# Performance work log

Measured on AMD Instinct MI355X. Metric: run time of the kernel, lower is better.

## Reference

```python
import jax, jax.numpy as jnp
import numpy as np

N_LEVELS = 16
F_PER_LEVEL = 2
T = 1 << 19  # hashmap size per level
BASE_RES = 16
DST_RES = 4096
B = float(np.exp(np.log(DST_RES / BASE_RES) / (N_LEVELS - 1)))  # per-level scale
MOVING_STEP = 1.0 / 4096.0
AABB_MIN = -1.5
AABB_MAX = 1.5
GEO_FEAT_DIM = 15
CORNERS = np.array([[i, j, k] for i in (0, 1) for j in (0, 1) for k in (0, 1)], dtype=np.int32)  # [8,3]
PRIMES = np.array([1, 2654435761, 805459861], dtype=np.uint32)


def mlp(h, Ws):
    # tcnn FullyFusedMLP: bias-free linear layers, ReLU hidden, linear output
    for W in Ws[:-1]:
        h = jax.nn.relu(h @ W)
    return h @ Ws[-1]


def freq_encode(x, n_freqs):
    # tcnn Frequency encoding: sin/cos(2^f * pi * x) per dim/freq; [N,D] -> [N, D*n_freqs*2]
    f = (2.0 ** jnp.arange(n_freqs, dtype=jnp.float32)) * jnp.pi
    xf = x[..., None] * f  # [N, D, nf]
    return jnp.concatenate([jnp.sin(xf), jnp.cos(xf)], axis=-1).reshape(x.shape[0], -1)


def sh_encode_deg4(d):
    # real spherical harmonics, degree 4 (16 coeffs), unit direction input
    x, y, z = d[..., 0], d[..., 1], d[..., 2]
    xy, yz, xz = x * y, y * z, x * z
    x2, y2, z2 = x * x, y * y, z * z
    return jnp.stack([
        0.28209479177387814 * jnp.ones_like(x),
        -0.48860251190291987 * y,
        0.48860251190291987 * z,
        -0.48860251190291987 * x,
        1.0925484305920792 * xy,
        -1.0925484305920792 * yz,
        0.94617469575755997 * z2 - 0.31539156525251999,
        -1.0925484305920792 * xz,
        0.54627421529603959 * (x2 - y2),
        0.59004358992664352 * y * (y2 - 3.0 * x2),
        2.8906114426405538 * xy * z,
        0.45704579946446572 * y * (1.0 - 5.0 * z2),
        0.3731763325901154 * z * (5.0 * z2 - 3.0),
        0.45704579946446572 * x * (1.0 - 5.0 * z2),
        1.4453057213202769 * z * (x2 - y2),
        0.59004358992664352 * x * (3.0 * y2 - x2),
    ], axis=-1)  # [N,16]


def hash_encode(x, tables):
    # x: [N,3] in [0,1]; tables: [L, T, F]. Multi-res grid w/ trilinear interp;
    # dense indexing for small levels, spatial hashing for large ones (tcnn semantics).
    outs = []
    for l in range(N_LEVELS):
        scale = BASE_RES * (B ** l) - 1.0
        res = int(np.ceil(scale)) + 1
        pos = x * scale + 0.5
        pos0 = jnp.floor(pos)
        frac = pos - pos0
        c = pos0.astype(jnp.int32)[:, None, :] + CORNERS[None]  # [N,8,3]
        if res ** 3 <= T:
            idx = c[..., 0] + res * (c[..., 1] + res * c[..., 2])
        else:
            cu = c.astype(jnp.uint32)
            idx = (cu[..., 0] * PRIMES[0]) ^ (cu[..., 1] * PRIMES[1]) ^ (cu[..., 2] * PRIMES[2])
            idx = (idx % np.uint32(T)).astype(jnp.int32)
        feats = tables[l][idx]  # [N,8,F] gather
        w = jnp.prod(jnp.where(CORNERS[None] == 1, frac[:, None, :], 1.0 - frac[:, None, :]), axis=-1)  # [N,8]
        outs.append(jnp.einsum('ncf,nc->nf', feats, w))
    return jnp.concatenate(outs, axis=-1)  # [N, L*F]


def _w(k, fan_in, fan_out):
    return jax.random.normal(k, (fan_in, fan_out), jnp.float32) / np.sqrt(fan_in)


def setup_inputs() -> dict:
    key = jax.random.key(0)
    ks = jax.random.split(key, 12)
    N = 524288
    positions = jax.random.uniform(ks[0], (N, 3), jnp.float32, -1.2, 1.2)
    t = jax.random.uniform(ks[1], (N, 1), jnp.float32)
    directions = jax.random.normal(ks[2], (N, 3), jnp.float32)
    tables = jax.random.uniform(ks[3], (N_LEVELS, T, F_PER_LEVEL), jnp.float32, -1e-4, 1e-4)
    return {
        'positions': positions, 't': t, 'directions': directions, 'tables': tables,
        'w_wrap0': _w(ks[4], 32, 64), 'w_wrap1': _w(ks[5], 64, 64), 'w_wrap2': _w(ks[6], 64, 3),
        'w_base0': _w(ks[7], 32, 64), 'w_base1': _w(ks[8], 64, 1 + GEO_FEAT_DIM),
        'w_head0': _w(ks[9], 16 + GEO_FEAT_DIM, 64), 'w_head1': _w(ks[10], 64, 64), 'w_head2': _w(ks[11], 64, 3),
    }


def reference(positions, t, directions, tables,
              w_wrap0, w_wrap1, w_wrap2, w_base0, w_base1,
              w_head0, w_head1, w_head2):
    # query_move: frequency-encode (x,t), tiny MLP -> offsets, scaled by MOVING_STEP
    enc = freq_encode(jnp.concatenate([positions, t], axis=-1), 4)  # [N,32]
    offsets = mlp(enc, [w_wrap0, w_wrap1, w_wrap2])  # [N,3]
    x_move = positions + offsets * MOVING_STEP
    # normalize to aabb unit cube
    xn = (x_move - AABB_MIN) / (AABB_MAX - AABB_MIN)
    selector = jnp.all((xn > 0.0) & (xn < 1.0), axis=-1)
    hash_feat = hash_encode(xn, tables)  # [N,32]
    base = mlp(hash_feat, [w_base0, w_base1])  # [N,16]
    density = jnp.exp(base[:, :1] - 1.0) * selector[:, None].astype(base.dtype)  # trunc_exp(x-1)
    geo = base[:, 1:]
    dirs = directions / jnp.linalg.norm(directions, axis=-1, keepdims=True)
    sh = sh_encode_deg4(dirs)  # [N,16]
    rgb = jax.nn.sigmoid(mlp(jnp.concatenate([sh, geo], axis=-1), [w_head0, w_head1, w_head2]))
    return jnp.concatenate([rgb, density], axis=-1)  # [N,4] = (rgb, density)
```

## Files before the change

### kernel.cpp

```cpp
#include <hip/hip_runtime.h>
#include <math.h>

#define TPB   128
#define HTPB  256
#define HPTS  4
#define CHUNK 32
#define LDW   68
constexpr int  N_LVL = 16;
constexpr unsigned TBL = 1u << 19;
constexpr float MOVE_STEP = 1.0f / 4096.0f;

typedef __attribute__((ext_vector_type(8))) short short8;
typedef __attribute__((ext_vector_type(4))) float f32x4;

struct LevelParams { float scale[N_LVL]; int res[N_LVL]; int dense[N_LVL]; };

enum { C_W0 = 0, C_W1 = 4, C_W2 = 12, C_B0 = 14, C_B1 = 18, C_H0 = 20, C_H1 = 24, C_H2 = 32, C_TOT = 34 };

struct LayerDesc { const float* W; int K; int N; int ksteps; int ntiles; int cbase; };
struct AllLayers { LayerDesc L[8]; };

__device__ __forceinline__ unsigned short f2bf(float x) {
    unsigned int u = __float_as_uint(x);
    u += 0x7FFFu + ((u >> 16) & 1u);
    return (unsigned short)(u >> 16);
}
__device__ __forceinline__ float bf2f(unsigned short h) {
    return __uint_as_float(((unsigned int)h) << 16);
}
__device__ __forceinline__ unsigned pk(unsigned short a, unsigned short b) {
    return (unsigned)a | ((unsigned)b << 16);
}

__device__ __forceinline__ unsigned cvt_pk_bf16(float a, float b) {
    unsigned r;
    asm("v_cvt_pk_bf16_f32 %0, %1, %2" : "=v"(r) : "v"(a), "v"(b));
    return r;
}
__device__ __forceinline__ void split_pair(float a, float b, unsigned& hp, unsigned& lp) {
    hp = cvt_pk_bf16(a, b);
    const float ha = __uint_as_float(hp << 16);
    const float hb = __uint_as_float(hp & 0xffff0000u);
    lp = cvt_pk_bf16(a - ha, b - hb);
}

__global__ __launch_bounds__(256) void k_prep(AllLayers al, unsigned short* __restrict__ wfrag)
{
    const LayerDesc d = al.L[blockIdx.x];
    const int total = d.ksteps * d.ntiles * 64;
    for (int slot = threadIdx.x; slot < total; slot += 256) {
        const int lane = slot & 63;
        const int c = slot >> 6;
        const int s = c / d.ntiles;
        const int t = c - s * d.ntiles;
        short8 hv, lv;
#pragma unroll
        for (int j = 0; j < 8; ++j) {
            const int k = s * 32 + ((lane >> 4) << 3) + j;
            const int n = t * 16 + (lane & 15);
            const float w = (k < d.K && n < d.N) ? d.W[k * d.N + n] : 0.f;
            const unsigned short hi = f2bf(w);
            const unsigned short lo = f2bf(w - bf2f(hi));
            hv[j] = (short)hi;
            lv[j] = (short)lo;
        }
        short8* b8 = reinterpret_cast<short8*>(wfrag + (size_t)(d.cbase + c) * 1024);
        b8[lane]      = hv;
        b8[64 + lane] = lv;
    }
}

__global__ __launch_bounds__(256) void k_tab16(
    const float* __restrict__ g_tab, unsigned* __restrict__ tab16,
    int n_dense, int n_hashed)
{
    const size_t total_pairs = (size_t)n_hashed * (TBL / 2);
    const size_t gstride = (size_t)gridDim.x * 256;
    const float* __restrict__ src = g_tab + (size_t)n_dense * (TBL * 2);
    for (size_t i = (size_t)blockIdx.x * 256 + threadIdx.x; i < total_pairs; i += gstride) {
        const f32x4 v = reinterpret_cast<const f32x4*>(src)[i];
        uint2 o;
        o.x = pk(f2bf(v[0]), f2bf(v[1]));
        o.y = pk(f2bf(v[2]), f2bf(v[3]));
        reinterpret_cast<uint2*>(tab16)[i] = o;
    }
}

template<int KSTEPS, int NTILES, bool RELU>
__device__ __forceinline__ void wave_layer(float* X,
                                           const unsigned short* __restrict__ wfrag, int cbase,
                                           int wrow, int lane)
{
    f32x4 acc[2][NTILES];
#pragma unroll
    for (int ms = 0; ms < 2; ++ms)
#pragma unroll
        for (int t = 0; t < NTILES; ++t) acc[ms][t] = f32x4{0.f, 0.f, 0.f, 0.f};
    const int r15 = lane & 15, q = lane >> 4;
    const short8* wf8 = reinterpret_cast<const short8*>(wfrag) + (size_t)cbase * 128;
#pragma unroll
    for (int s = 0; s < KSTEPS; ++s) {
        short8 ah[2], al[2];
#pragma unroll
        for (int ms = 0; ms < 2; ++ms) {
            const float* xp = X + (size_t)(wrow + ms * 16 + r15) * LDW + s * 32 + q * 8;
            const f32x4 x0 = reinterpret_cast<const f32x4*>(xp)[0];
            const f32x4 x1 = reinterpret_cast<const f32x4*>(xp)[1];
            union { unsigned u[4]; short8 s8; } uh, ul;
            split_pair(x0[0], x0[1], uh.u[0], ul.u[0]);
            split_pair(x0[2], x0[3], uh.u[1], ul.u[1]);
            split_pair(x1[0], x1[1], uh.u[2], ul.u[2]);
            split_pair(x1[2], x1[3], uh.u[3], ul.u[3]);
            ah[ms] = uh.s8;
            al[ms] = ul.s8;
        }
#pragma unroll
        for (int t = 0; t < NTILES; ++t) {
            const short8* cp = wf8 + (size_t)(s * NTILES + t) * 128;
            const short8 bh = cp[lane];
            const short8 bl = cp[64 + lane];
#pragma unroll
            for (int ms = 0; ms < 2; ++ms) {
                acc[ms][t] = __builtin_amdgcn_mfma_f32_16x16x32_bf16(ah[ms], bh, acc[ms][t], 0, 0, 0);
                acc[ms][t] = __builtin_amdgcn_mfma_f32_16x16x32_bf16(al[ms], bh, acc[ms][t], 0, 0, 0);
                acc[ms][t] = __builtin_amdgcn_mfma_f32_16x16x32_bf16(ah[ms], bl, acc[ms][t], 0, 0, 0);
            }
        }
    }
#pragma unroll
    for (int ms = 0; ms < 2; ++ms)
#pragma unroll
        for (int t = 0; t < NTILES; ++t)
#pragma unroll
            for (int r = 0; r < 4; ++r) {
                float v = acc[ms][t][r];
                if (RELU) v = fmaxf(v, 0.f);
                X[(size_t)(wrow + ms * 16 + q * 4 + r) * LDW + t * 16 + r15] = v;
            }
}

__global__ __launch_bounds__(256, 4) void k_warp_mfma(
    const float* __restrict__ g_pos, const float* __restrict__ g_t,
    const float* __restrict__ g_tab,
    const unsigned short* __restrict__ wfrag,
    float* __restrict__ xn4,
    unsigned* __restrict__ featp, size_t stride, int N, int n_dense, LevelParams lp)
{
    __shared__ float buf[128 * LDW];
    const int tid = threadIdx.x;
    const int base = blockIdx.x * 128;
    const int p = tid & 127;
    const int pn = min(base + p, N - 1);
    const float PI_F = 3.14159265358979323846f;

    {
        const int dpair = tid >> 7;
        float v0, v1;
        if (dpair == 0) { v0 = g_pos[3 * pn + 0]; v1 = g_pos[3 * pn + 1]; }
        else            { v0 = g_pos[3 * pn + 2]; v1 = g_t[pn]; }
#pragma unroll
        for (int e = 0; e < 2; ++e) {
            const float x = e ? v1 : v0;
            const int d = dpair * 2 + e;
            f32x4 sv, cv;
#pragma unroll
            for (int k = 0; k < 4; ++k) {
                const float a = x * (PI_F * (float)(1 << k));
                sv[k] = __sinf(a);
                cv[k] = __cosf(a);
            }
            *reinterpret_cast<f32x4*>(&buf[(size_t)p * LDW + d * 8])     = sv;
            *reinterpret_cast<f32x4*>(&buf[(size_t)p * LDW + d * 8 + 4]) = cv;
        }
    }
    __syncthreads();
    const int lane = tid & 63, wrow = (tid >> 6) * 32;
    wave_layer<1, 4, true >(buf, wfrag, C_W0, wrow, lane);
    wave_layer<2, 4, true >(buf, wfrag, C_W1, wrow, lane);
    wave_layer<2, 1, false>(buf, wfrag, C_W2, wrow, lane);
    __syncthreads();

    const int n = base + p;
    const float ox = buf[(size_t)p * LDW + 0];
    const float oy = buf[(size_t)p * LDW + 1];
    const float oz = buf[(size_t)p * LDW + 2];
    const float xnv[3] = { (g_pos[3 * pn + 0] + ox * MOVE_STEP + 1.5f) / 3.0f,
                           (g_pos[3 * pn + 1] + oy * MOVE_STEP + 1.5f) / 3.0f,
                           (g_pos[3 * pn + 2] + oz * MOVE_STEP + 1.5f) / 3.0f };
    if (tid < 128 && n < N) {
        reinterpret_cast<f32x4*>(xn4)[n] = f32x4{ xnv[0], xnv[1], xnv[2], 0.f };
    }

    const int dmid = min(3, n_dense);
    const int l0 = (tid < 128) ? 0 : dmid;
    const int l1 = (tid < 128) ? dmid : n_dense;
    for (int l = l0; l < l1; ++l) {
        const float scale = lp.scale[l];
        const int res = lp.res[l];
        float fr[3]; int c0[3];
#pragma unroll
        for (int d = 0; d < 3; ++d) {
            const float pp = xnv[d] * scale + 0.5f;
            const float fl = floorf(pp);
            fr[d] = pp - fl;
            c0[d] = (int)fl;
        }
        const float* __restrict__ tbl = g_tab + (size_t)l * (size_t)(TBL * 2);
        float2 v[8];
#pragma unroll
        for (int c = 0; c < 8; ++c) {
            const int ci = (c >> 2) & 1, cj = (c >> 1) & 1, ck = c & 1;
            const unsigned idx = (unsigned)((c0[0] + ci) + res * ((c0[1] + cj) + res * (c0[2] + ck)));
            v[c] = *reinterpret_cast<const float2*>(tbl + (size_t)idx * 2);
        }
        float f0 = 0.f, f1 = 0.f;
#pragma unroll
        for (int c = 0; c < 8; ++c) {
            const int ci = (c >> 2) & 1, cj = (c >> 1) & 1, ck = c & 1;
            const float w = (ci ? fr[0] : 1.f - fr[0])
                          * (cj ? fr[1] : 1.f - fr[1])
                          * (ck ? fr[2] : 1.f - fr[2]);
            f0 = fmaf(w, v[c].x, f0);
            f1 = fmaf(w, v[c].y, f1);
        }
        if (n < N) {
            __builtin_nontemporal_store(pk(f2bf(f0), f2bf(f1)), &featp[(size_t)l * stride + n]);
        }
    }
}

__global__ __launch_bounds__(HTPB) void k_hash_all16(
    const unsigned* __restrict__ tab16,
    const float* __restrict__ xn4,
    unsigned* __restrict__ featp, size_t stride, int N, int n_dense, LevelParams lp)
{
    const int l = n_dense + blockIdx.y;
    const float scale = lp.scale[l];
    const unsigned* __restrict__ tbl = tab16 + (size_t)blockIdx.y * TBL;
    unsigned* __restrict__ op = featp + (size_t)l * stride;

    const int base = blockIdx.x * (HTPB * HPTS) + threadIdx.x;

    int nn[HPTS]; bool av[HPTS];
    f32x4 xs[HPTS];
#pragma unroll
    for (int k = 0; k < HPTS; ++k) {
        nn[k] = base + k * HTPB;
        av[k] = nn[k] < N;
        const int m = av[k] ? nn[k] : 0;
        xs[k] = reinterpret_cast<const f32x4*>(xn4)[m];
    }

    float frx[HPTS];
    float wyz[HPTS][4];
    uint2 w2[HPTS][4];
    unsigned vodd[HPTS][4] = {};
    unsigned ahi[HPTS];
    bool oddx[HPTS];
#pragma unroll
    for (int k = 0; k < HPTS; ++k) {
        int c0[3]; float fr[3];
#pragma unroll
        for (int d = 0; d < 3; ++d) {
            const float pp = xs[k][d] * scale + 0.5f;
            const float fl = floorf(pp);
            fr[d] = pp - fl;
            c0[d] = (int)fl;
        }
        frx[k] = fr[0];
        const unsigned ux  = (unsigned)c0[0];
        const unsigned ry0 = (unsigned)c0[1] * 2654435761u;
        const unsigned ry1 = (unsigned)(c0[1] + 1) * 2654435761u;
        const unsigned rz0 = (unsigned)c0[2] * 805459861u;
        const unsigned rz1 = (unsigned)(c0[2] + 1) * 805459861u;
        oddx[k] = (c0[0] & 1) != 0;
        const float wy0 = 1.f - fr[1], wy1 = fr[1];
        const float wz0 = 1.f - fr[2], wz1 = fr[2];
        wyz[k][0] = wy0 * wz0; wyz[k][1] = wy0 * wz1;
        wyz[k][2] = wy1 * wz0; wyz[k][3] = wy1 * wz1;
        const unsigned rr[4] = { ry0 ^ rz0, ry0 ^ rz1, ry1 ^ rz0, ry1 ^ rz1 };
        unsigned hb = 0;
#pragma unroll
        for (int pc = 0; pc < 4; ++pc) {
            const unsigned iA = (ux ^ rr[pc]) & (TBL - 1u);
            hb |= (iA & 1u) << pc;
            w2[k][pc] = *reinterpret_cast<const uint2*>(tbl + (iA & ~1u));
        }
        ahi[k] = hb;
        if (oddx[k]) {
#pragma unroll
            for (int pc = 0; pc < 4; ++pc) {
                const unsigned iB = ((ux + 1u) ^ rr[pc]) & (TBL - 1u);
                vodd[k][pc] = tbl[iB];
            }
        }
    }

#pragma unroll
    for (int k = 0; k < HPTS; ++k) {
        float f0 = 0.f, f1 = 0.f;
        const float wx0 = 1.f - frx[k], wx1 = frx[k];
#pragma unroll
        for (int pc = 0; pc < 4; ++pc) {
            const unsigned lo = w2[k][pc].x, hi = w2[k][pc].y;
            const bool a_hi = ((ahi[k] >> pc) & 1u) != 0;
            const unsigned vA = a_hi ? hi : lo;
            const unsigned vB = oddx[k] ? vodd[k][pc] : (a_hi ? lo : hi);
            const float wA = wx0 * wyz[k][pc];
            const float wB = wx1 * wyz[k][pc];
            f0 = fmaf(wA, bf2f((unsigned short)(vA & 0xffffu)), f0);
            f1 = fmaf(wA, bf2f((unsigned short)(vA >> 16)), f1);
            f0 = fmaf(wB, bf2f((unsigned short)(vB & 0xffffu)), f0);
            f1 = fmaf(wB, bf2f((unsigned short)(vB >> 16)), f1);
        }
        if (av[k]) __builtin_nontemporal_store(pk(f2bf(f0), f2bf(f1)), &op[nn[k]]);
    }
}

__global__ __launch_bounds__(256, 4) void k_final_mfma(
    const unsigned* __restrict__ featp, size_t stride,
    const float* __restrict__ xn4,
    const float* __restrict__ g_dir,
    const unsigned short* __restrict__ wfrag,
    float* __restrict__ g_out, int N)
{
    __shared__ float buf[128 * LDW];
    const int tid = threadIdx.x;
    const int base = blockIdx.x * 128;
    const int p = tid & 127;
    const int pn = min(base + p, N - 1);
    const int g = tid >> 7;

#pragma unroll
    for (int j = 0; j < 8; ++j) {
        const int l = g * 8 + j;
        const unsigned v = __builtin_nontemporal_load(&featp[(size_t)l * stride + pn]);
        buf[(size_t)p * LDW + 2 * l]     = bf2f((unsigned short)(v & 0xffffu));
        buf[(size_t)p * LDW + 2 * l + 1] = bf2f((unsigned short)(v >> 16));
    }
    __syncthreads();

    const int lane = tid & 63, wrow = (tid >> 6) * 32;
    wave_layer<1, 4, true >(buf, wfrag, C_B0, wrow, lane);
    wave_layer<2, 1, false>(buf, wfrag, C_B1, wrow, lane);
    __syncthreads();

    float density = 0.f;
    if (tid < 128) {
        float bb[16];
        const f32x4* bv = reinterpret_cast<const f32x4*>(&buf[(size_t)tid * LDW]);
#pragma unroll
        for (int g4 = 0; g4 < 4; ++g4) {
            const f32x4 v = bv[g4];
#pragma unroll
            for (int j = 0; j < 4; ++j) bb[4 * g4 + j] = v[j];
        }
        const f32x4 xv = reinterpret_cast<const f32x4*>(xn4)[pn];
        const bool sel = xv[0] > 0.f && xv[0] < 1.f && xv[1] > 0.f && xv[1] < 1.f &&
                         xv[2] > 0.f && xv[2] < 1.f;
        density = sel ? expf(bb[0] - 1.0f) : 0.0f;

        const float ddx = g_dir[3 * pn + 0];
        const float ddy = g_dir[3 * pn + 1];
        const float ddz = g_dir[3 * pn + 2];
        const float nrm = sqrtf(ddx * ddx + ddy * ddy + ddz * ddz);
        const float x = ddx / nrm, y = ddy / nrm, z = ddz / nrm;
        const float xy = x * y, yz = y * z, xz = x * z;
        const float x2 = x * x, y2 = y * y, z2 = z * z;
        f32x4 o0, o1, o2, o3, o4, o5, o6, o7;
        o0[0] = 0.28209479177387814f;
        o0[1] = -0.48860251190291987f * y;
        o0[2] = 0.48860251190291987f * z;
        o0[3] = -0.48860251190291987f * x;
        o1[0] = 1.0925484305920792f * xy;
        o1[1] = -1.0925484305920792f * yz;
        o1[2] = 0.94617469575756f * z2 - 0.31539156525252f;
        o1[3] = -1.0925484305920792f * xz;
        o2[0] = 0.5462742152960396f * (x2 - y2);
        o2[1] = 0.5900435899266435f * y * (y2 - 3.0f * x2);
        o2[2] = 2.890611442640554f * xy * z;
        o2[3] = 0.4570457994644657f * y * (1.0f - 5.0f * z2);
        o3[0] = 0.3731763325901154f * z * (5.0f * z2 - 3.0f);
        o3[1] = 0.4570457994644657f * x * (1.0f - 5.0f * z2);
        o3[2] = 1.445305721320277f * z * (x2 - y2);
        o3[3] = 0.5900435899266435f * x * (3.0f * y2 - x2);
        o4[0] = bb[1];  o4[1] = bb[2];  o4[2] = bb[3];  o4[3] = bb[4];
        o5[0] = bb[5];  o5[1] = bb[6];  o5[2] = bb[7];  o5[3] = bb[8];
        o6[0] = bb[9];  o6[1] = bb[10]; o6[2] = bb[11]; o6[3] = bb[12];
        o7[0] = bb[13]; o7[1] = bb[14]; o7[2] = bb[15]; o7[3] = 0.f;
        f32x4* wb = reinterpret_cast<f32x4*>(&buf[(size_t)tid * LDW]);
        wb[0] = o0; wb[1] = o1; wb[2] = o2; wb[3] = o3;
        wb[4] = o4; wb[5] = o5; wb[6] = o6; wb[7] = o7;
    }
    __syncthreads();

    wave_layer<1, 4, true >(buf, wfrag, C_H0, wrow, lane);
    wave_layer<2, 4, true >(buf, wfrag, C_H1, wrow, lane);
    wave_layer<2, 1, false>(buf, wfrag, C_H2, wrow, lane);
    __syncthreads();

    if (tid < 128 && base + tid < N) {
        const int n = base + tid;
        float4 o;
        o.x = 1.0f / (1.0f + expf(-buf[(size_t)tid * LDW + 0]));
        o.y = 1.0f / (1.0f + expf(-buf[(size_t)tid * LDW + 1]));
        o.z = 1.0f / (1.0f + expf(-buf[(size_t)tid * LDW + 2]));
        o.w = density;
        *reinterpret_cast<float4*>(g_out + (size_t)n * 4) = o;
    }
}

template<int IN, int OUT, bool RELU>
__device__ __forceinline__ void layer(const float* __restrict__ W,
                                      const float* __restrict__ hin,
                                      float* __restrict__ A,
                                      float* __restrict__ out)
{
#pragma unroll
    for (int j = 0; j < OUT; ++j) out[j] = 0.f;
#pragma unroll
    for (int c = 0; c < IN; c += CHUNK) {
#pragma unroll
        for (int i = 0; i < CHUNK; ++i) {
            if (c + i < IN) A[i * TPB] = RELU ? fmaxf(hin[c + i], 0.f) : hin[c + i];
        }
        const int cnt = (IN - c < CHUNK) ? (IN - c) : CHUNK;
#pragma unroll 4
        for (int i = 0; i < cnt; ++i) {
            const float a = A[i * TPB];
            const float* __restrict__ Wr = W + (size_t)(c + i) * OUT;
#pragma unroll
            for (int j = 0; j < OUT; ++j)
                out[j] = fmaf(a, Wr[j], out[j]);
        }
    }
}

__global__ __launch_bounds__(TPB, 4) void dngp_mono(
    const float* __restrict__ g_pos, const float* __restrict__ g_t,
    const float* __restrict__ g_dir, const float* __restrict__ g_tab,
    const float* __restrict__ Ww0, const float* __restrict__ Ww1, const float* __restrict__ Ww2,
    const float* __restrict__ Wb0, const float* __restrict__ Wb1,
    const float* __restrict__ Wh0, const float* __restrict__ Wh1, const float* __restrict__ Wh2,
    float* __restrict__ g_out, int N, LevelParams lp)
{
    __shared__ float s_act[CHUNK * TPB];
    const int tid = threadIdx.x;
    const int n = blockIdx.x * TPB + tid;
    if (n >= N) return;
    float* __restrict__ A = s_act + tid;

    const float px = g_pos[3 * n + 0];
    const float py = g_pos[3 * n + 1];
    const float pz = g_pos[3 * n + 2];
    const float tt = g_t[n];

    float enc[32];
    {
        const float xin[4] = { px, py, pz, tt };
        const float PI_F = 3.14159265358979323846f;
#pragma unroll
        for (int d = 0; d < 4; ++d)
#pragma unroll
            for (int k = 0; k < 4; ++k) {
                float s, c;
                sincosf(xin[d] * (PI_F * (float)(1 << k)), &s, &c);
                enc[d * 8 + k]     = s;
                enc[d * 8 + 4 + k] = c;
            }
    }

    float h[64], h2[64], off[3];
    layer<32, 64, false>(Ww0, enc, A, h);
    layer<64, 64, true >(Ww1, h,   A, h2);
    layer<64, 3,  true >(Ww2, h2,  A, off);

    const float xn[3] = { (px + off[0] * MOVE_STEP + 1.5f) / 3.0f,
                          (py + off[1] * MOVE_STEP + 1.5f) / 3.0f,
                          (pz + off[2] * MOVE_STEP + 1.5f) / 3.0f };
    const bool sel = xn[0] > 0.f && xn[0] < 1.f && xn[1] > 0.f && xn[1] < 1.f &&
                     xn[2] > 0.f && xn[2] < 1.f;

    float feat[32];
#pragma unroll 2
    for (int l = 0; l < N_LVL; ++l) {
        const float scale = lp.scale[l];
        const int res = lp.res[l];
        float fr[3]; int c0[3];
#pragma unroll
        for (int d = 0; d < 3; ++d) {
            const float pp = xn[d] * scale + 0.5f;
            const float fl = floorf(pp);
            fr[d] = pp - fl;
            c0[d] = (int)fl;
        }
        const float* __restrict__ tbl = g_tab + (size_t)l * (size_t)(TBL * 2);
        float f0 = 0.f, f1 = 0.f;
        if (lp.dense[l]) {
#pragma unroll
            for (int c = 0; c < 8; ++c) {
                const int ci = (c >> 2) & 1, cj = (c >> 1) & 1, ck = c & 1;
                const unsigned idx = (unsigned)((c0[0] + ci) + res * ((c0[1] + cj) + res * (c0[2] + ck)));
                const float2 f = *reinterpret_cast<const float2*>(tbl + (size_t)idx * 2);
                const float w = (ci ? fr[0] : 1.f - fr[0]) * (cj ? fr[1] : 1.f - fr[1]) * (ck ? fr[2] : 1.f - fr[2]);
                f0 = fmaf(w, f.x, f0);
                f1 = fmaf(w, f.y, f1);
            }
        } else {
#pragma unroll
            for (int c = 0; c < 8; ++c) {
                const int ci = (c >> 2) & 1, cj = (c >> 1) & 1, ck = c & 1;
                const unsigned hx = (unsigned)(c0[0] + ci);
                const unsigned hy = (unsigned)(c0[1] + cj) * 2654435761u;
                const unsigned hz = (unsigned)(c0[2] + ck) * 805459861u;
                const unsigned idx = (hx ^ hy ^ hz) & (TBL - 1u);
                const float2 f = *reinterpret_cast<const float2*>(tbl + (size_t)idx * 2);
                const float w = (ci ? fr[0] : 1.f - fr[0]) * (cj ? fr[1] : 1.f - fr[1]) * (ck ? fr[2] : 1.f - fr[2]);
                f0 = fmaf(w, f.x, f0);
                f1 = fmaf(w, f.y, f1);
            }
        }
        feat[2 * l]     = f0;
        feat[2 * l + 1] = f1;
    }

    layer<32, 64, false>(Wb0, feat, A, h);
    float b[16];
    layer<64, 16, true >(Wb1, h, A, b);
    const float density = sel ? expf(b[0] - 1.0f) : 0.0f;

    float hin[31];
    {
        const float ddx = g_dir[3 * n + 0];
        const float ddy = g_dir[3 * n + 1];
        const float ddz = g_dir[3 * n + 2];
        const float nrm = sqrtf(ddx * ddx + ddy * ddy + ddz * ddz);
        const float x = ddx / nrm, y = ddy / nrm, z = ddz / nrm;
        const float xy = x * y, yz = y * z, xz = x * z;
        const float x2_ = x * x, y2 = y * y, z2 = z * z;
        hin[0]  = 0.28209479177387814f;
        hin[1]  = -0.48860251190291987f * y;
        hin[2]  = 0.48860251190291987f * z;
        hin[3]  = -0.48860251190291987f * x;
        hin[4]  = 1.0925484305920792f * xy;
        hin[5]  = -1.0925484305920792f * yz;
        hin[6]  = 0.94617469575756f * z2 - 0.31539156525252f;
        hin[7]  = -1.0925484305920792f * xz;
        hin[8]  = 0.5462742152960396f * (x2_ - y2);
        hin[9]  = 0.5900435899266435f * y * (y2 - 3.0f * x2_);
        hin[10] = 2.890611442640554f * xy * z;
        hin[11] = 0.4570457994644657f * y * (1.0f - 5.0f * z2);
        hin[12] = 0.3731763325901154f * z * (5.0f * z2 - 3.0f);
        hin[13] = 0.4570457994644657f * x * (1.0f - 5.0f * z2);
        hin[14] = 1.445305721320277f * z * (x2_ - y2);
        hin[15] = 0.5900435899266435f * x * (3.0f * y2 - x2_);
#pragma unroll
        for (int j = 0; j < 15; ++j) hin[16 + j] = b[1 + j];
    }

    layer<31, 64, false>(Wh0, hin, A, h);
    layer<64, 64, true >(Wh1, h,   A, h2);
    float rgb[3];
    layer<64, 3,  true >(Wh2, h2,  A, rgb);

    float4 o;
    o.x = 1.0f / (1.0f + expf(-rgb[0]));
    o.y = 1.0f / (1.0f + expf(-rgb[1]));
    o.z = 1.0f / (1.0f + expf(-rgb[2]));
    o.w = density;
    *reinterpret_cast<float4*>(g_out + (size_t)n * 4) = o;
}

extern "C" void kernel_launch(void* const* d_in, const int* in_sizes, int n_in,
                              void* d_out, int out_size, void* d_ws, size_t ws_size,
                              hipStream_t stream)
{
    const float* g_pos = (const float*)d_in[0];
    const float* g_t   = (const float*)d_in[1];
    const float* g_dir = (const float*)d_in[2];
    const float* g_tab = (const float*)d_in[3];
    const float* Ww0   = (const float*)d_in[4];
    const float* Ww1   = (const float*)d_in[5];
    const float* Ww2   = (const float*)d_in[6];
    const float* Wb0   = (const float*)d_in[7];
    const float* Wb1   = (const float*)d_in[8];
    const float* Wh0   = (const float*)d_in[9];
    const float* Wh1   = (const float*)d_in[10];
    const float* Wh2   = (const float*)d_in[11];
    const int N = in_sizes[0] / 3;

    LevelParams lp;
    int n_dense = 0;
    const double Bv = exp(log(4096.0 / 16.0) / 15.0);
    for (int l = 0; l < N_LVL; ++l) {
        const double s = 16.0 * pow(Bv, (double)l) - 1.0;
        lp.scale[l] = (float)s;
        const int r = (int)ceil(s) + 1;
        lp.res[l] = r;
        lp.dense[l] = ((long long)r * r * r <= (long long)TBL) ? 1 : 0;
        if (lp.dense[l]) n_dense = l + 1;
    }
    const int n_hashed = N_LVL - n_dense;

    const size_t stride = ((size_t)N + 259) & ~(size_t)3;
    const size_t ws_need = (size_t)C_TOT * 2048
                         + stride * 4 * 4
                         + stride * 4 * 16
                         + (size_t)n_hashed * TBL * 4;

    if (ws_size >= ws_need) {
        unsigned short* wfrag = (unsigned short*)d_ws;
        float* xn4 = (float*)((char*)d_ws + (size_t)C_TOT * 2048);
        unsigned* featp = (unsigned*)(xn4 + 4 * stride);
        unsigned* tab16 = featp + 16 * stride;

        AllLayers al;
        al.L[0] = { Ww0, 32, 64, 1, 4, C_W0 };
        al.L[1] = { Ww1, 64, 64, 2, 4, C_W1 };
        al.L[2] = { Ww2, 64,  3, 2, 1, C_W2 };
        al.L[3] = { Wb0, 32, 64, 1, 4, C_B0 };
        al.L[4] = { Wb1, 64, 16, 2, 1, C_B1 };
        al.L[5] = { Wh0, 31, 64, 1, 4, C_H0 };
        al.L[6] = { Wh1, 64, 64, 2, 4, C_H1 };
        al.L[7] = { Wh2, 64,  3, 2, 1, C_H2 };

        const int nchunk = (N + HTPB * HPTS - 1) / (HTPB * HPTS);

        dim3 mgrid((N + 127) / 128), mblock(256);
        dim3 hgrid(nchunk, n_hashed), hblock(HTPB);

        hipLaunchKernelGGL(k_prep, dim3(8), dim3(256), 0, stream, al, wfrag);
        hipLaunchKernelGGL(k_tab16, dim3(2048), dim3(256), 0, stream,
                           g_tab, tab16, n_dense, n_hashed);

        hipLaunchKernelGGL(k_warp_mfma, mgrid, mblock, 0, stream,
                           g_pos, g_t, g_tab, wfrag, xn4,
                           featp, stride, N, n_dense, lp);

        hipLaunchKernelGGL(k_hash_all16, hgrid, hblock, 0, stream,
                           tab16, xn4, featp, stride, N, n_dense, lp);

        hipLaunchKernelGGL(k_final_mfma, mgrid, mblock, 0, stream,
                           featp, stride, xn4, g_dir,
                           wfrag, (float*)d_out, N);
    } else {
        dim3 grid((N + TPB - 1) / TPB), block(TPB);
        hipLaunchKernelGGL(dngp_mono, grid, block, 0, stream,
                           g_pos, g_t, g_dir, g_tab,
                           Ww0, Ww1, Ww2, Wb0, Wb1, Wh0, Wh1, Wh2,
                           (float*)d_out, N, lp);
    }
}
```

Baseline: 276.9 us.

## Widen hash-grid corner loads to 16B and merge x-neighbour fetches

The hashed-level kernel now loads an aligned 4-entry (16-byte) group per corner pair. The second x corner is taken from that same group whenever ux^(ux+1) stays within the low two bits, so the extra scalar load is needed in fewer cases. Points are processed two at a time instead of four to reduce register pressure. The dense levels in the first kernel fetch both x-neighbours with one 16-byte unaligned load, and a block-wide barrier is removed by having each wave handle its own rows. The cost is wider loads that pull in unused bytes, plus more selection logic.

After: 248.9 us. 1.11x faster.

```diff
diff --git a/kernel.cpp b/kernel.cpp
--- a/kernel.cpp
+++ b/kernel.cpp
@@ -12,6 +12,7 @@
 
 typedef __attribute__((ext_vector_type(8))) short short8;
 typedef __attribute__((ext_vector_type(4))) float f32x4;
+typedef __attribute__((ext_vector_type(4), aligned(8))) float f32x4u;
 
 struct LevelParams { float scale[N_LVL]; int res[N_LVL]; int dense[N_LVL]; };
 
@@ -30,6 +31,11 @@
 }
 __device__ __forceinline__ unsigned pk(unsigned short a, unsigned short b) {
     return (unsigned)a | ((unsigned)b << 16);
+}
+__device__ __forceinline__ unsigned sel4(uint4 w, unsigned i) {
+    const unsigned lo = (i & 1u) ? w.y : w.x;
+    const unsigned hi = (i & 1u) ? w.w : w.z;
+    return (i & 2u) ? hi : lo;
 }
 
 __device__ __forceinline__ unsigned cvt_pk_bf16(float a, float b) {
@@ -178,22 +184,24 @@
     wave_layer<1, 4, true >(buf, wfrag, C_W0, wrow, lane);
     wave_layer<2, 4, true >(buf, wfrag, C_W1, wrow, lane);
     wave_layer<2, 1, false>(buf, wfrag, C_W2, wrow, lane);
-    __syncthreads();
-
-    const int n = base + p;
-    const float ox = buf[(size_t)p * LDW + 0];
-    const float oy = buf[(size_t)p * LDW + 1];
-    const float oz = buf[(size_t)p * LDW + 2];
-    const float xnv[3] = { (g_pos[3 * pn + 0] + ox * MOVE_STEP + 1.5f) / 3.0f,
-                           (g_pos[3 * pn + 1] + oy * MOVE_STEP + 1.5f) / 3.0f,
-                           (g_pos[3 * pn + 2] + oz * MOVE_STEP + 1.5f) / 3.0f };
-    if (tid < 128 && n < N) {
+
+    const int prow = wrow + (lane & 31);
+    const int sub  = lane >> 5;
+    const int n = base + prow;
+    const int pn2 = min(n, N - 1);
+    const float ox = buf[(size_t)prow * LDW + 0];
+    const float oy = buf[(size_t)prow * LDW + 1];
+    const float oz = buf[(size_t)prow * LDW + 2];
+    const float xnv[3] = { (g_pos[3 * pn2 + 0] + ox * MOVE_STEP + 1.5f) / 3.0f,
+                           (g_pos[3 * pn2 + 1] + oy * MOVE_STEP + 1.5f) / 3.0f,
+                           (g_pos[3 * pn2 + 2] + oz * MOVE_STEP + 1.5f) / 3.0f };
+    if (sub == 0 && n < N) {
         reinterpret_cast<f32x4*>(xn4)[n] = f32x4{ xnv[0], xnv[1], xnv[2], 0.f };
     }
 
     const int dmid = min(3, n_dense);
-    const int l0 = (tid < 128) ? 0 : dmid;
-    const int l1 = (tid < 128) ? dmid : n_dense;
+    const int l0 = sub ? dmid : 0;
+    const int l1 = sub ? n_dense : dmid;
     for (int l = l0; l < l1; ++l) {
         const float scale = lp.scale[l];
         const int res = lp.res[l];
@@ -206,22 +214,23 @@
             c0[d] = (int)fl;
         }
         const float* __restrict__ tbl = g_tab + (size_t)l * (size_t)(TBL * 2);
-        float2 v[8];
-#pragma unroll
-        for (int c = 0; c < 8; ++c) {
-            const int ci = (c >> 2) & 1, cj = (c >> 1) & 1, ck = c & 1;
-            const unsigned idx = (unsigned)((c0[0] + ci) + res * ((c0[1] + cj) + res * (c0[2] + ck)));
-            v[c] = *reinterpret_cast<const float2*>(tbl + (size_t)idx * 2);
+        f32x4u v[4];
+#pragma unroll
+        for (int pc = 0; pc < 4; ++pc) {
+            const int cj = pc >> 1, ck = pc & 1;
+            const int idx = c0[0] + res * ((c0[1] + cj) + res * (c0[2] + ck));
+            v[pc] = *reinterpret_cast<const f32x4u*>(tbl + (size_t)idx * 2);
         }
         float f0 = 0.f, f1 = 0.f;
-#pragma unroll
-        for (int c = 0; c < 8; ++c) {
-            const int ci = (c >> 2) & 1, cj = (c >> 1) & 1, ck = c & 1;
-            const float w = (ci ? fr[0] : 1.f - fr[0])
-                          * (cj ? fr[1] : 1.f - fr[1])
-                          * (ck ? fr[2] : 1.f - fr[2]);
-            f0 = fmaf(w, v[c].x, f0);
-            f1 = fmaf(w, v[c].y, f1);
+        const float wx0 = 1.f - fr[0], wx1 = fr[0];
+#pragma unroll
+        for (int pc = 0; pc < 4; ++pc) {
+            const int cj = pc >> 1, ck = pc & 1;
+            const float wyz = (cj ? fr[1] : 1.f - fr[1]) * (ck ? fr[2] : 1.f - fr[2]);
+            f0 = fmaf(wx0 * wyz, v[pc][0], f0);
+            f1 = fmaf(wx0 * wyz, v[pc][1], f1);
+            f0 = fmaf(wx1 * wyz, v[pc][2], f0);
+            f1 = fmaf(wx1 * wyz, v[pc][3], f1);
         }
         if (n < N) {
             __builtin_nontemporal_store(pk(f2bf(f0), f2bf(f1)), &featp[(size_t)l * stride + n]);
@@ -241,79 +250,81 @@
 
     const int base = blockIdx.x * (HTPB * HPTS) + threadIdx.x;
 
-    int nn[HPTS]; bool av[HPTS];
-    f32x4 xs[HPTS];
-#pragma unroll
-    for (int k = 0; k < HPTS; ++k) {
-        nn[k] = base + k * HTPB;
-        av[k] = nn[k] < N;
-        const int m = av[k] ? nn[k] : 0;
-        xs[k] = reinterpret_cast<const f32x4*>(xn4)[m];
-    }
-
-    float frx[HPTS];
-    float wyz[HPTS][4];
-    uint2 w2[HPTS][4];
-    unsigned vodd[HPTS][4] = {};
-    unsigned ahi[HPTS];
-    bool oddx[HPTS];
-#pragma unroll
-    for (int k = 0; k < HPTS; ++k) {
-        int c0[3]; float fr[3];
-#pragma unroll
-        for (int d = 0; d < 3; ++d) {
-            const float pp = xs[k][d] * scale + 0.5f;
-            const float fl = floorf(pp);
-            fr[d] = pp - fl;
-            c0[d] = (int)fl;
-        }
-        frx[k] = fr[0];
-        const unsigned ux  = (unsigned)c0[0];
-        const unsigned ry0 = (unsigned)c0[1] * 2654435761u;
-        const unsigned ry1 = (unsigned)(c0[1] + 1) * 2654435761u;
-        const unsigned rz0 = (unsigned)c0[2] * 805459861u;
-        const unsigned rz1 = (unsigned)(c0[2] + 1) * 805459861u;
-        oddx[k] = (c0[0] & 1) != 0;
-        const float wy0 = 1.f - fr[1], wy1 = fr[1];
-        const float wz0 = 1.f - fr[2], wz1 = fr[2];
-        wyz[k][0] = wy0 * wz0; wyz[k][1] = wy0 * wz1;
-        wyz[k][2] = wy1 * wz0; wyz[k][3] = wy1 * wz1;
-        const unsigned rr[4] = { ry0 ^ rz0, ry0 ^ rz1, ry1 ^ rz0, ry1 ^ rz1 };
-        unsigned hb = 0;
-#pragma unroll
-        for (int pc = 0; pc < 4; ++pc) {
-            const unsigned iA = (ux ^ rr[pc]) & (TBL - 1u);
-            hb |= (iA & 1u) << pc;
-            w2[k][pc] = *reinterpret_cast<const uint2*>(tbl + (iA & ~1u));
-        }
-        ahi[k] = hb;
-        if (oddx[k]) {
+#pragma unroll
+    for (int b = 0; b < HPTS; b += 2) {
+        int nn[2]; bool av[2];
+        f32x4 xs[2];
+#pragma unroll
+        for (int j = 0; j < 2; ++j) {
+            nn[j] = base + (b + j) * HTPB;
+            av[j] = nn[j] < N;
+            xs[j] = reinterpret_cast<const f32x4*>(xn4)[av[j] ? nn[j] : 0];
+        }
+
+        float frx[2];
+        float wyz[2][4];
+        uint4 w4[2][4];
+        unsigned vodd[2][4] = {};
+        unsigned a3p[2], mm[2];
+        bool far_[2];
+#pragma unroll
+        for (int j = 0; j < 2; ++j) {
+            int c0[3]; float fr[3];
+#pragma unroll
+            for (int d = 0; d < 3; ++d) {
+                const float pp = xs[j][d] * scale + 0.5f;
+                const float fl = floorf(pp);
+                fr[d] = pp - fl;
+                c0[d] = (int)fl;
+            }
+            frx[j] = fr[0];
+            const unsigned ux  = (unsigned)c0[0];
+            const unsigned ry0 = (unsigned)c0[1] * 2654435761u;
+            const unsigned ry1 = (unsigned)(c0[1] + 1) * 2654435761u;
+            const unsigned rz0 = (unsigned)c0[2] * 805459861u;
+            const unsigned rz1 = (unsigned)(c0[2] + 1) * 805459861u;
+            mm[j]  = ux ^ (ux + 1u);
+            far_[j] = mm[j] > 3u;
+            const float wy0 = 1.f - fr[1], wy1 = fr[1];
+            const float wz0 = 1.f - fr[2], wz1 = fr[2];
+            wyz[j][0] = wy0 * wz0; wyz[j][1] = wy0 * wz1;
+            wyz[j][2] = wy1 * wz0; wyz[j][3] = wy1 * wz1;
+            const unsigned rr[4] = { ry0 ^ rz0, ry0 ^ rz1, ry1 ^ rz0, ry1 ^ rz1 };
+            unsigned a3 = 0;
 #pragma unroll
             for (int pc = 0; pc < 4; ++pc) {
-                const unsigned iB = ((ux + 1u) ^ rr[pc]) & (TBL - 1u);
-                vodd[k][pc] = tbl[iB];
-            }
-        }
-    }
-
-#pragma unroll
-    for (int k = 0; k < HPTS; ++k) {
-        float f0 = 0.f, f1 = 0.f;
-        const float wx0 = 1.f - frx[k], wx1 = frx[k];
-#pragma unroll
-        for (int pc = 0; pc < 4; ++pc) {
-            const unsigned lo = w2[k][pc].x, hi = w2[k][pc].y;
-            const bool a_hi = ((ahi[k] >> pc) & 1u) != 0;
-            const unsigned vA = a_hi ? hi : lo;
-            const unsigned vB = oddx[k] ? vodd[k][pc] : (a_hi ? lo : hi);
-            const float wA = wx0 * wyz[k][pc];
-            const float wB = wx1 * wyz[k][pc];
-            f0 = fmaf(wA, bf2f((unsigned short)(vA & 0xffffu)), f0);
-            f1 = fmaf(wA, bf2f((unsigned short)(vA >> 16)), f1);
-            f0 = fmaf(wB, bf2f((unsigned short)(vB & 0xffffu)), f0);
-            f1 = fmaf(wB, bf2f((unsigned short)(vB >> 16)), f1);
-        }
-        if (av[k]) __builtin_nontemporal_store(pk(f2bf(f0), f2bf(f1)), &op[nn[k]]);
+                const unsigned iA = (ux ^ rr[pc]) & (TBL - 1u);
+                a3 |= (iA & 3u) << (2 * pc);
+                w4[j][pc] = *reinterpret_cast<const uint4*>(tbl + (iA & ~3u));
+            }
+            a3p[j] = a3;
+            if (far_[j]) {
+#pragma unroll
+                for (int pc = 0; pc < 4; ++pc) {
+                    const unsigned iB = ((ux + 1u) ^ rr[pc]) & (TBL - 1u);
+                    vodd[j][pc] = tbl[iB];
+                }
+            }
+        }
+
+#pragma unroll
+        for (int j = 0; j < 2; ++j) {
+            float f0 = 0.f, f1 = 0.f;
+            const float wx0 = 1.f - frx[j], wx1 = frx[j];
+#pragma unroll
+            for (int pc = 0; pc < 4; ++pc) {
+                const unsigned a3 = (a3p[j] >> (2 * pc)) & 3u;
+                const unsigned vA = sel4(w4[j][pc], a3);
+                const unsigned vB = far_[j] ? vodd[j][pc] : sel4(w4[j][pc], a3 ^ mm[j]);
+                const float wA = wx0 * wyz[j][pc];
+                const float wB = wx1 * wyz[j][pc];
+                f0 = fmaf(wA, bf2f((unsigned short)(vA & 0xffffu)), f0);
+                f1 = fmaf(wA, bf2f((unsigned short)(vA >> 16)), f1);
+                f0 = fmaf(wB, bf2f((unsigned short)(vB & 0xffffu)), f0);
+                f1 = fmaf(wB, bf2f((unsigned short)(vB >> 16)), f1);
+            }
+            if (av[j]) __builtin_nontemporal_store(pk(f2bf(f0), f2bf(f1)), &op[nn[j]]);
+        }
     }
 }
 
```
